# Performance work log

Hardware: AMD Instinct MI355X
Metric: run time of the kernel (lower is better)

Reference implementation:

```python
import jax, jax.numpy as jnp
import numpy as np

DIM = 256
HEADS = 8
HEAD_DIM = DIM // HEADS
EDGE_TYPES = 8  # edge_type_count; table has EDGE_TYPES+1 rows, row 0 is padding
B, N = 2, 2048
EPS = 1e-5


def layer_norm(x, g, b):
    mu = jnp.mean(x, axis=-1, keepdims=True)
    var = jnp.mean(jnp.square(x - mu), axis=-1, keepdims=True)
    return (x - mu) * jax.lax.rsqrt(var + EPS) * g + b


def setup_inputs() -> dict:
    key = jax.random.key(0)
    ks = jax.random.split(key, 12)
    s = 0.02
    x = jax.random.normal(ks[0], (B, N, DIM), dtype=jnp.float32)
    edge_types = jax.random.randint(ks[1], (B, N, N), 0, EDGE_TYPES + 1, dtype=jnp.int32)
    node_mask = jax.random.randint(ks[2], (B, N), 0, 2, dtype=jnp.int32).astype(bool)
    qkv_w = jax.random.normal(ks[3], (DIM, 3 * DIM), dtype=jnp.float32) * s
    qkv_b = jnp.zeros((3 * DIM,), jnp.float32)
    proj_w = jax.random.normal(ks[4], (DIM, DIM), dtype=jnp.float32) * s
    proj_b = jnp.zeros((DIM,), jnp.float32)
    edge_bias_table = jax.random.normal(ks[5], (EDGE_TYPES + 1, HEADS), dtype=jnp.float32) * s
    edge_bias_table = edge_bias_table.at[0].set(0.0)  # padding_idx=0
    ln1_g = jnp.ones((DIM,), jnp.float32); ln1_b = jnp.zeros((DIM,), jnp.float32)
    ln2_g = jnp.ones((DIM,), jnp.float32); ln2_b = jnp.zeros((DIM,), jnp.float32)
    ffn_w1 = jax.random.normal(ks[6], (DIM, 4 * DIM), dtype=jnp.float32) * s
    ffn_b1 = jnp.zeros((4 * DIM,), jnp.float32)
    ffn_w2 = jax.random.normal(ks[7], (4 * DIM, DIM), dtype=jnp.float32) * s
    ffn_b2 = jnp.zeros((DIM,), jnp.float32)
    return dict(x=x, edge_types=edge_types, node_mask=node_mask,
                qkv_w=qkv_w, qkv_b=qkv_b, proj_w=proj_w, proj_b=proj_b,
                edge_bias_table=edge_bias_table, ln1_g=ln1_g, ln1_b=ln1_b,
                ln2_g=ln2_g, ln2_b=ln2_b, ffn_w1=ffn_w1, ffn_b1=ffn_b1,
                ffn_w2=ffn_w2, ffn_b2=ffn_b2)


def reference(x, edge_types, node_mask, qkv_w, qkv_b, proj_w, proj_b,
              edge_bias_table, ln1_g, ln1_b, ln2_g, ln2_b,
              ffn_w1, ffn_b1, ffn_w2, ffn_b2):
    scale = HEAD_DIM ** -0.5
    residual = x
    h = layer_norm(x, ln1_g, ln1_b)
    qkv = h @ qkv_w + qkv_b                         # [B,N,3*DIM]
    qkv = qkv.reshape(B, N, 3, HEADS, HEAD_DIM)
    q, k, v = (qkv[:, :, 0].transpose(0, 2, 1, 3),  # [B,H,N,d]
               qkv[:, :, 1].transpose(0, 2, 1, 3),
               qkv[:, :, 2].transpose(0, 2, 1, 3))
    scores = jnp.einsum('bhnd,bhmd->bhnm', q, k) * scale
    bias = edge_bias_table[edge_types]              # [B,N,N,H]
    scores = scores + bias.transpose(0, 3, 1, 2)    # [B,H,N,N]
    eye = jnp.eye(N, dtype=bool)
    edge_mask = (edge_types != 0) | eye[None]
    node_mask_2d = node_mask[:, None, :] & node_mask[:, :, None]
    attn_mask = edge_mask & node_mask_2d            # [B,N,N]
    scores = jnp.where(attn_mask[:, None], scores, -1e9)
    attn = jax.nn.softmax(scores, axis=-1)
    out = jnp.einsum('bhnm,bhmd->bhnd', attn, v)
    out = out.transpose(0, 2, 1, 3).reshape(B, N, DIM)
    out = (out @ proj_w + proj_b) * node_mask[:, :, None]
    x1 = residual + out
    h2 = layer_norm(x1, ln2_g, ln2_b)
    h2 = jax.nn.gelu(h2 @ ffn_w1 + ffn_b1, approximate=False) @ ffn_w2 + ffn_b2
    h2 = h2 * node_mask[:, :, None]
    return x1 + h2
```

## Files before the change

### kernel.cpp

```cpp
#include <hip/hip_runtime.h>
#include <math.h>

#define DIMM 256
#define HEADS 8
#define NB 2048
#define BB 2
#define ROWS (BB*NB)

typedef __attribute__((ext_vector_type(8))) short bf16x8;
typedef __attribute__((ext_vector_type(4))) short bf16x4;
typedef __attribute__((ext_vector_type(4))) float f32x4;

__device__ inline unsigned short f2bf(float f) {
    unsigned int u = __float_as_uint(f);
    u += 0x7FFFu + ((u >> 16) & 1u);
    return (unsigned short)(u >> 16);
}
__device__ inline float bf2f(unsigned short u) {
    return __uint_as_float(((unsigned int)u) << 16);
}

__device__ inline int get_mask(const void* nm, int fmt, int idx) {
    if (fmt) return ((const unsigned char*)nm)[idx] != 0;
    return ((const int*)nm)[idx] != 0;
}

__global__ __launch_bounds__(256) void scan_w2bft_kernel(
    const void* __restrict__ nmask, int* __restrict__ nv,
    unsigned short* __restrict__ qidx,
    const float* __restrict__ w0, const float* __restrict__ w1,
    const float* __restrict__ w2, const float* __restrict__ w3,
    unsigned short* __restrict__ o0, unsigned short* __restrict__ o1,
    unsigned short* __restrict__ o2, unsigned short* __restrict__ o3)
{
    __shared__ float tile[64][65];
    __shared__ int fsh;
    __shared__ int cnt[256];
    int bid = blockIdx.x, t = threadIdx.x;
    if (bid < BB) {
        if (t == 0) fsh = 0;
        __syncthreads();
        if (((const unsigned char*)nmask)[4 * t + 1] != 0) fsh = 1;
        __syncthreads();
        int fm = fsh;
        int b = bid;
        int m[8]; int c = 0;
#pragma unroll
        for (int i = 0; i < 8; ++i) {
            m[i] = get_mask(nmask, fm, b * NB + t * 8 + i);
            c += m[i];
        }
        cnt[t] = c;
        __syncthreads();
#pragma unroll
        for (int off = 1; off < 256; off <<= 1) {
            int v = (t >= off) ? cnt[t - off] : 0;
            __syncthreads();
            cnt[t] += v;
            __syncthreads();
        }
        int mybase = cnt[t] - c;
        if (t == 255) nv[b] = cnt[255];
        int off = mybase;
#pragma unroll
        for (int i = 0; i < 8; ++i) {
            int row = t * 8 + i;
            if (m[i]) qidx[b * NB + off++] = (unsigned short)row;
        }
        __syncthreads();
        if (t == 0) {
            int n = cnt[255];
            unsigned short last = (n > 0) ? qidx[b * NB + n - 1] : (unsigned short)0;
            int padend = (n + 63) & ~63;
            for (int i = n; i < padend; ++i) qidx[b * NB + i] = last;
        }
    } else {
        int wb = bid - BB;
        const float* src; unsigned short* dst; int K, N, idx;
        if (wb < 48)       { src = w0; dst = o0; K = 256;  N = 768;  idx = wb; }
        else if (wb < 64)  { src = w1; dst = o1; K = 256;  N = 256;  idx = wb - 48; }
        else if (wb < 128) { src = w2; dst = o2; K = 256;  N = 1024; idx = wb - 64; }
        else               { src = w3; dst = o3; K = 1024; N = 256;  idx = wb - 128; }
        int ntiles = N >> 6;
        int k0 = (idx / ntiles) * 64, n0 = (idx % ntiles) * 64;
        int r = t >> 4, c4 = (t & 15) * 4;
#pragma unroll
        for (int i = 0; i < 4; ++i) {
            float4 v = *(const float4*)&src[(size_t)(k0 + r + i * 16) * N + n0 + c4];
            tile[r + i * 16][c4 + 0] = v.x;
            tile[r + i * 16][c4 + 1] = v.y;
            tile[r + i * 16][c4 + 2] = v.z;
            tile[r + i * 16][c4 + 3] = v.w;
        }
        __syncthreads();
#pragma unroll
        for (int i = 0; i < 4; ++i) {
            int n = n0 + r + i * 16;
            ushort4 u;
            u.x = f2bf(tile[c4 + 0][r + i * 16]);
            u.y = f2bf(tile[c4 + 1][r + i * 16]);
            u.z = f2bf(tile[c4 + 2][r + i * 16]);
            u.w = f2bf(tile[c4 + 3][r + i * 16]);
            *(ushort4*)&dst[(size_t)n * K + k0 + c4] = u;
        }
    }
}

__device__ inline void ln8_body(const float* __restrict__ x, const float* __restrict__ g,
                                const float* __restrict__ bb, unsigned short* __restrict__ o,
                                int xrow, int orow, int lane32) {
    int c0 = lane32 * 8;
    float4 v0 = *(const float4*)&x[(size_t)xrow * DIMM + c0];
    float4 v1 = *(const float4*)&x[(size_t)xrow * DIMM + c0 + 4];
    float s  = v0.x + v0.y + v0.z + v0.w + v1.x + v1.y + v1.z + v1.w;
    float s2 = v0.x*v0.x + v0.y*v0.y + v0.z*v0.z + v0.w*v0.w
             + v1.x*v1.x + v1.y*v1.y + v1.z*v1.z + v1.w*v1.w;
#pragma unroll
    for (int off = 16; off >= 1; off >>= 1) {
        s  += __shfl_xor(s,  off);
        s2 += __shfl_xor(s2, off);
    }
    float mean = s * (1.0f / DIMM);
    float var  = s2 * (1.0f / DIMM) - mean * mean;
    float rstd = rsqrtf(var + 1e-5f);
    float4 g0 = *(const float4*)&g[c0],  g1 = *(const float4*)&g[c0 + 4];
    float4 b0 = *(const float4*)&bb[c0], b1 = *(const float4*)&bb[c0 + 4];
    ushort4 u0, u1;
    u0.x = f2bf((v0.x - mean) * rstd * g0.x + b0.x);
    u0.y = f2bf((v0.y - mean) * rstd * g0.y + b0.y);
    u0.z = f2bf((v0.z - mean) * rstd * g0.z + b0.z);
    u0.w = f2bf((v0.w - mean) * rstd * g0.w + b0.w);
    u1.x = f2bf((v1.x - mean) * rstd * g1.x + b1.x);
    u1.y = f2bf((v1.y - mean) * rstd * g1.y + b1.y);
    u1.z = f2bf((v1.z - mean) * rstd * g1.z + b1.z);
    u1.w = f2bf((v1.w - mean) * rstd * g1.w + b1.w);
    *(ushort4*)&o[(size_t)orow * DIMM + c0]     = u0;
    *(ushort4*)&o[(size_t)orow * DIMM + c0 + 4] = u1;
}

__global__ __launch_bounds__(256) void prep_kernel(
    const float* __restrict__ x, const float* __restrict__ ln1_g,
    const float* __restrict__ ln1_b, unsigned short* __restrict__ h_ln,
    const int* __restrict__ etypes,
    unsigned char* __restrict__ emaskP,
    const int* __restrict__ nv, const unsigned short* __restrict__ qidx)
{
    __shared__ unsigned short kq[4][64];
    int bid = blockIdx.x, t = threadIdx.x;
    if (bid < 512) {
        int slotg = bid * 8 + (t >> 5);
        int b = slotg >> 11, sl = slotg & 2047;
        int nvp = (nv[b] + 63) & ~63;
        if (sl < nvp) {
            int row = qidx[b * NB + sl];
            ln8_body(x, ln1_g, ln1_b, h_ln, b * NB + row, slotg, t & 31);
        }
    } else {
        int wu = t >> 6;
        int unit = (bid - 512) * 4 + wu;
        int lane = t & 63, quad = lane >> 4, l15 = lane & 15;
        int b = unit >> 12;
        int qt16 = (unit >> 5) & 127;
        int kt = unit & 31;
        int nvb = nv[b];
        int nvp = (nvb + 63) & ~63;
        if (qt16 * 16 >= nvb || kt * 64 >= nvp) return;
        kq[wu][lane] = qidx[b * NB + kt * 64 + lane];
        int slot = qt16 * 16 + l15;
        int validq = slot < nvb;
        int qr = qidx[b * NB + slot];
        const int* erow = etypes + (size_t)(b * NB + qr) * NB;
        unsigned int dw[2] = {0u, 0u};
#pragma unroll
        for (int t16 = 0; t16 < 4; ++t16) {
            ushort4 ko = *(const ushort4*)&kq[wu][t16 * 16 + quad * 4];
            unsigned short kos[4] = {ko.x, ko.y, ko.z, ko.w};
#pragma unroll
            for (int r = 0; r < 4; ++r) {
                int ks = kt * 64 + t16 * 16 + quad * 4 + r;
                unsigned int code = 0u;
                if (validq && ks < nvb) {
                    int korig = kos[r];
                    int et = erow[korig];
                    if ((et != 0) || (korig == qr)) code = (unsigned int)(et + 1);
                }
                dw[t16 >> 1] |= code << ((t16 & 1) * 16 + r * 4);
            }
        }
        int2 o = {(int)dw[0], (int)dw[1]};
        *(int2*)(emaskP + (size_t)unit * 512 + lane * 8) = o;
    }
}

__global__ __launch_bounds__(256) void gemm_qkv_mfma(
    const unsigned short* __restrict__ A, const unsigned short* __restrict__ Bt,
    const float* __restrict__ bias, const int* __restrict__ nv,
    unsigned short* __restrict__ qkvh, unsigned short* __restrict__ vT)
{
    const int K = 256;
    int t = threadIdx.x, w = t >> 6, l = t & 63;
    int l15 = l & 15, quad = l >> 4;
    int n0 = blockIdx.x * 64;
    int m0c = blockIdx.y * 64;
    int b = blockIdx.z;
    int nvp = (nv[b] + 63) & ~63;
    if (m0c >= nvp) return;
    const unsigned short* ap = A + (size_t)(b * NB + m0c + w * 16 + l15) * K + quad * 8;
    const unsigned short* bp = Bt + (size_t)(n0 + l15) * K + quad * 8;

    f32x4 acc[4];
#pragma unroll
    for (int c = 0; c < 4; ++c) acc[c] = (f32x4){0.f, 0.f, 0.f, 0.f};

    bf16x8 aA, bA[4], aB, bB[4];
    auto ld = [&](bf16x8& af, bf16x8 (&bf)[4], int k0) {
        af = *(const bf16x8*)(ap + k0);
#pragma unroll
        for (int c = 0; c < 4; ++c)
            bf[c] = *(const bf16x8*)(bp + (size_t)(c * 16) * K + k0);
    };
    auto pr = [&](const bf16x8& af, const bf16x8 (&bf)[4]) {
#pragma unroll
        for (int c = 0; c < 4; ++c)
            acc[c] = __builtin_amdgcn_mfma_f32_16x16x32_bf16(af, bf[c], acc[c], 0, 0, 0);
    };
    ld(aA, bA, 0);
    for (int k0 = 0; k0 < K; k0 += 64) {
        ld(aB, bB, k0 + 32);
        pr(aA, bA);
        if (k0 + 64 < K) ld(aA, bA, k0 + 64);
        pr(aB, bB);
    }

    if (n0 < 512) {
        float sc = (n0 < 256) ? 0.17677669529663689f : 1.0f;
#pragma unroll
        for (int r = 0; r < 4; ++r) {
            int slot = b * NB + m0c + w * 16 + quad * 4 + r;
#pragma unroll
            for (int c = 0; c < 4; ++c) {
                int col = n0 + c * 16 + l15;
                qkvh[(size_t)slot * 512 + col] = f2bf((acc[c][r] + bias[col]) * sc);
            }
        }
    } else {
        int n = m0c + w * 16 + quad * 4;
#pragma unroll
        for (int c = 0; c < 4; ++c) {
            int col = n0 + c * 16 + l15 - 512;
            int hidx = col >> 5, d = col & 31;
            float bs = bias[n0 + c * 16 + l15];
            ushort4 u;
            u.x = f2bf(acc[c][0] + bs);
            u.y = f2bf(acc[c][1] + bs);
            u.z = f2bf(acc[c][2] + bs);
            u.w = f2bf(acc[c][3] + bs);
            *(ushort4*)&vT[(size_t)((b * HEADS + hidx) * 32 + d) * NB + n] = u;
        }
    }
}

__global__ __launch_bounds__(256) void attn_mfma(
    const unsigned short* __restrict__ qkvh,
    const unsigned short* __restrict__ vT,
    const unsigned char* __restrict__ emaskP,
    const float* __restrict__ table,
    const int* __restrict__ nv,
    unsigned short* __restrict__ OpH, float* __restrict__ lpart)
{
    __shared__ unsigned short P[4][16][72];
    __shared__ float tab2m[16];

    int t = threadIdx.x;
    int w = t >> 6, l = t & 63;
    int l15 = l & 15, quad = l >> 4;
    int h = blockIdx.x;
    int qt = blockIdx.y;
    int z = blockIdx.z, b = z >> 2, sp = z & 3;

    if (t < 16) tab2m[t] = (t >= 1 && t < 10) ? __expf(table[(t - 1) * 8 + h]) : 0.f;
    __syncthreads();

    int nvb = nv[b];
    int qt16 = qt * 4 + w;
    int q0c = qt16 * 16;
    if (q0c >= nvb) return;

    int nkt = (nvb + 63) >> 6;
    int tps = (nkt + 3) >> 2;
    int kbase = sp * tps * 64;
    int kend = min(kbase + tps * 64, nkt * 64);

    bf16x8 bq = *(const bf16x8*)(qkvh + (size_t)(b * NB + q0c + l15) * 512 + h * 32 + quad * 8);

    const unsigned short* kp = qkvh + (size_t)(b * NB + l15) * 512 + 256 + h * 32 + quad * 8;
    const unsigned short* vp = vT + (size_t)((b * HEADS + h) * 32 + l15) * NB + quad * 8;
    const unsigned char* ep = emaskP + (size_t)((b * 128 + qt16) * 32) * 512 + l * 8;

    float lacc = 0.f;
    f32x4 O0 = {0.f, 0.f, 0.f, 0.f}, O1 = {0.f, 0.f, 0.f, 0.f};

    bf16x8 kA[4], kB[4];
    bf16x8 vA[2][2], vB[2][2];
    int2 eA, eB;

    auto loadtile = [&](bf16x8 (&kf)[4], bf16x8 (&vf)[2][2], int2& ef, int m0) {
#pragma unroll
        for (int t16 = 0; t16 < 4; ++t16)
            kf[t16] = *(const bf16x8*)(kp + (size_t)(m0 + t16 * 16) * 512);
#pragma unroll
        for (int ks = 0; ks < 2; ++ks) {
            vf[ks][0] = *(const bf16x8*)(vp + m0 + ks * 32);
            vf[ks][1] = *(const bf16x8*)(vp + 16 * NB + m0 + ks * 32);
        }
        ef = *(const int2*)(ep + (size_t)(m0 >> 6) * 512);
    };

    auto process = [&](const bf16x8 (&kf)[4], const bf16x8 (&vf)[2][2], const int2& ef) {
#pragma unroll
        for (int t16 = 0; t16 < 4; ++t16) {
            f32x4 zero = {0.f, 0.f, 0.f, 0.f};
            f32x4 sT = __builtin_amdgcn_mfma_f32_16x16x32_bf16(kf[t16], bq, zero, 0, 0, 0);
            unsigned int e = ((unsigned int)((t16 < 2) ? ef.x : ef.y)) >> ((t16 & 1) * 16);
            float p0 = __expf(sT[0]) * tab2m[e & 0xFu];
            float p1 = __expf(sT[1]) * tab2m[(e >> 4) & 0xFu];
            float p2 = __expf(sT[2]) * tab2m[(e >> 8) & 0xFu];
            float p3 = __expf(sT[3]) * tab2m[(e >> 12) & 0xFu];
            lacc += (p0 + p1) + (p2 + p3);
            bf16x4 pb;
            pb[0] = (short)f2bf(p0); pb[1] = (short)f2bf(p1);
            pb[2] = (short)f2bf(p2); pb[3] = (short)f2bf(p3);
            *(bf16x4*)&P[w][l15][t16 * 16 + quad * 4] = pb;
        }
#pragma unroll
        for (int ks = 0; ks < 2; ++ks) {
            bf16x8 pa = *(const bf16x8*)&P[w][l15][ks * 32 + quad * 8];
            O0 = __builtin_amdgcn_mfma_f32_16x16x32_bf16(pa, vf[ks][0], O0, 0, 0, 0);
            O1 = __builtin_amdgcn_mfma_f32_16x16x32_bf16(pa, vf[ks][1], O1, 0, 0, 0);
        }
    };

    if (kbase < kend) {
        loadtile(kA, vA, eA, kbase);
        for (int m0 = kbase; m0 < kend; m0 += 128) {
            int n1 = (m0 + 64 < kend) ? m0 + 64 : kbase;
            loadtile(kB, vB, eB, n1);
            process(kA, vA, eA);
            if (m0 + 128 < kend) loadtile(kA, vA, eA, m0 + 128);
            if (m0 + 64 < kend) process(kB, vB, eB);
        }
    }

    lacc += __shfl_xor(lacc, 16);
    lacc += __shfl_xor(lacc, 32);

    unsigned short* Ob = OpH + (size_t)sp * ROWS * DIMM;
#pragma unroll
    for (int r = 0; r < 4; ++r) {
        int slot = q0c + quad * 4 + r;
        if (slot < nvb) {
            Ob[(size_t)(b * NB + slot) * DIMM + h * 32 + l15]      = f2bf(O0[r]);
            Ob[(size_t)(b * NB + slot) * DIMM + h * 32 + 16 + l15] = f2bf(O1[r]);
        }
    }
    if (quad == 0 && q0c + l15 < nvb)
        lpart[(size_t)sp * ROWS * 8 + (size_t)(b * NB + q0c + l15) * 8 + h] = lacc;
}

__global__ __launch_bounds__(1024) void megaback(
    const unsigned short* __restrict__ OpH, const float* __restrict__ lpart,
    const unsigned short* __restrict__ projT, const float* __restrict__ proj_b,
    const float* __restrict__ x, const void* __restrict__ nmask,
    const float* __restrict__ g2, const float* __restrict__ b2,
    const unsigned short* __restrict__ f1T, const float* __restrict__ ffn_b1,
    const unsigned short* __restrict__ f2T, const float* __restrict__ ffn_b2,
    const int* __restrict__ nv, const unsigned short* __restrict__ qidx,
    float* __restrict__ out)
{
    __shared__ float rinv_l[16][8];
    __shared__ float stats[16][2];
    __shared__ float redn[16][16][2];
    __shared__ unsigned short Astage[16][264];
    __shared__ float x1s[16][260];
    __shared__ unsigned short hstage[16][264];
    __shared__ unsigned short midstage[16][1032];
    __shared__ int fsh;

    int t = threadIdx.x;
    int bid = blockIdx.x;

    if (bid >= 256) {
        if (t == 0) fsh = 0;
        __syncthreads();
        if (((const unsigned char*)nmask)[4 * t + 1] != 0) fsh = 1;
        __syncthreads();
        int fm = fsh;
        int row = (bid - 256) * 32 + (t >> 5);
        if (!get_mask(nmask, fm, row)) {
            int c0 = (t & 31) * 8;
            float4 v0 = *(const float4*)&x[(size_t)row * DIMM + c0];
            float4 v1 = *(const float4*)&x[(size_t)row * DIMM + c0 + 4];
            *(float4*)&out[(size_t)row * DIMM + c0]     = v0;
            *(float4*)&out[(size_t)row * DIMM + c0 + 4] = v1;
        }
        return;
    }

    int w = t >> 6, l = t & 63;
    int l15 = l & 15, quad = l >> 4;
    int b = bid >> 7;
    int s0 = (bid & 127) * 16;
    int nvb = nv[b];
    if (s0 >= nvb) return;
    int slot0 = b * NB + s0;
    int col = w * 16 + l15;

    const unsigned short* bpp = projT + (size_t)col * 256 + quad * 8;
    bf16x8 psb[4];
#pragma unroll
    for (int i = 0; i < 4; ++i) psb[i] = *(const bf16x8*)(bpp + i * 32);

    if (t < 128) {
        int row = t >> 3, h = t & 7;
        float s = 0.f;
#pragma unroll
        for (int sp = 0; sp < 4; ++sp)
            s += lpart[(size_t)sp * ROWS * 8 + (size_t)(slot0 + row) * 8 + h];
        rinv_l[row][h] = (s > 0.f) ? 1.f / s : 0.f;
    }
    __syncthreads();

    {
        int row = t >> 6, col4 = (t & 63) * 4;
        float rinv = rinv_l[row][col4 >> 5];
        float o0 = 0.f, o1 = 0.f, o2 = 0.f, o3 = 0.f;
#pragma unroll
        for (int sp = 0; sp < 4; ++sp) {
            ushort4 u = *(const ushort4*)&OpH[(size_t)sp * ROWS * DIMM +
                                             (size_t)(slot0 + row) * DIMM + col4];
            o0 += bf2f(u.x); o1 += bf2f(u.y); o2 += bf2f(u.z); o3 += bf2f(u.w);
        }
        ushort4 u;
        u.x = f2bf(o0 * rinv); u.y = f2bf(o1 * rinv);
        u.z = f2bf(o2 * rinv); u.w = f2bf(o3 * rinv);
        *(ushort4*)&Astage[row][col4] = u;
    }
    __syncthreads();

    {
        f32x4 acc = (f32x4){0.f, 0.f, 0.f, 0.f};
#pragma unroll
        for (int ch = 0; ch < 8; ++ch) {
            bf16x8 a = *(const bf16x8*)&Astage[l15][ch * 32 + quad * 8];
            acc = __builtin_amdgcn_mfma_f32_16x16x32_bf16(a, psb[ch & 3], acc, 0, 0, 0);
            if (ch + 4 < 8) psb[ch & 3] = *(const bf16x8*)(bpp + (ch + 4) * 32);
        }
        float bs = proj_b[col];
#pragma unroll
        for (int r = 0; r < 4; ++r) {
            int row = quad * 4 + r;
            int grow = b * NB + qidx[(size_t)(slot0 + row)];
            float v = (acc[r] + bs) + x[(size_t)grow * DIMM + col];
            x1s[row][col] = v;
            float s = v, s2 = v * v;
#pragma unroll
            for (int off = 1; off < 16; off <<= 1) {
                s += __shfl_xor(s, off); s2 += __shfl_xor(s2, off);
            }
            if (l15 == 0) { redn[row][w][0] = s; redn[row][w][1] = s2; }
        }
    }
    const unsigned short* bpf1 = f1T + (size_t)(w * 64 + l15) * 256 + quad * 8;
    bf16x8 f1A[4];
#pragma unroll
    for (int c = 0; c < 4; ++c) f1A[c] = *(const bf16x8*)(bpf1 + (size_t)(c * 16) * 256);
    __syncthreads();
    if (t < 16) {
        float s = 0.f, s2 = 0.f;
#pragma unroll
        for (int ww = 0; ww < 16; ++ww) { s += redn[t][ww][0]; s2 += redn[t][ww][1]; }
        float mean = s * (1.f / DIMM);
        float var  = s2 * (1.f / DIMM) - mean * mean;
        stats[t][0] = mean; stats[t][1] = rsqrtf(var + 1e-5f);
    }
    __syncthreads();

    {
        float gv = g2[col], bv = b2[col];
#pragma unroll
        for (int r = 0; r < 4; ++r) {
            int row = quad * 4 + r;
            float hv = (x1s[row][col] - stats[row][0]) * stats[row][1] * gv + bv;
            hstage[row][col] = f2bf(hv);
        }
    }
    __syncthreads();

    {
        f32x4 acc[4];
#pragma unroll
        for (int c = 0; c < 4; ++c) acc[c] = (f32x4){0.f, 0.f, 0.f, 0.f};
        bf16x8 bB[4];
#pragma unroll
        for (int ch = 0; ch < 8; ++ch) {
            bf16x8 a = *(const bf16x8*)&hstage[l15][ch * 32 + quad * 8];
            if (ch + 1 < 8) {
#pragma unroll
                for (int c = 0; c < 4; ++c)
                    bB[c] = *(const bf16x8*)(bpf1 + (size_t)(c * 16) * 256 + (ch + 1) * 32);
            }
#pragma unroll
            for (int c = 0; c < 4; ++c)
                acc[c] = __builtin_amdgcn_mfma_f32_16x16x32_bf16(a, f1A[c], acc[c], 0, 0, 0);
#pragma unroll
            for (int c = 0; c < 4; ++c) f1A[c] = bB[c];
        }
#pragma unroll
        for (int c = 0; c < 4; ++c) {
            int colf = w * 64 + c * 16 + l15;
            float bs = ffn_b1[colf];
#pragma unroll
            for (int r = 0; r < 4; ++r) {
                float v = acc[c][r] + bs;
                float x2 = v * v;
                float p = v * fmaf(0.07135481f, x2, 1.5957691f);
                float e = __expf(p);
                float gl = v * (e / (e + 1.f));
                midstage[quad * 4 + r][colf] = f2bf(gl);
            }
        }
    }
    const unsigned short* bpf2 = f2T + (size_t)col * 1024 + quad * 8;
    bf16x8 f2sb[4];
#pragma unroll
    for (int i = 0; i < 4; ++i) f2sb[i] = *(const bf16x8*)(bpf2 + i * 32);
    __syncthreads();

    {
        f32x4 acc = (f32x4){0.f, 0.f, 0.f, 0.f};
#pragma unroll
        for (int ch = 0; ch < 32; ++ch) {
            bf16x8 a = *(const bf16x8*)&midstage[l15][ch * 32 + quad * 8];
            acc = __builtin_amdgcn_mfma_f32_16x16x32_bf16(a, f2sb[ch & 3], acc, 0, 0, 0);
            if (ch + 4 < 32) f2sb[ch & 3] = *(const bf16x8*)(bpf2 + (ch + 4) * 32);
        }
        float bs = ffn_b2[col];
#pragma unroll
        for (int r = 0; r < 4; ++r) {
            int row = quad * 4 + r;
            if (s0 + row < nvb) {
                int grow = b * NB + qidx[(size_t)(slot0 + row)];
                out[(size_t)grow * DIMM + col] = x1s[row][col] + (acc[r] + bs);
            }
        }
    }
}

extern "C" void kernel_launch(void* const* d_in, const int* in_sizes, int n_in,
                              void* d_out, int out_size, void* d_ws, size_t ws_size,
                              hipStream_t stream) {
    const float* x       = (const float*)d_in[0];
    const int*   etypes  = (const int*)d_in[1];
    const void*  nmask   = d_in[2];
    const float* qkv_w   = (const float*)d_in[3];
    const float* qkv_b   = (const float*)d_in[4];
    const float* proj_w  = (const float*)d_in[5];
    const float* proj_b  = (const float*)d_in[6];
    const float* table   = (const float*)d_in[7];
    const float* ln1_g   = (const float*)d_in[8];
    const float* ln1_b   = (const float*)d_in[9];
    const float* ln2_g   = (const float*)d_in[10];
    const float* ln2_b   = (const float*)d_in[11];
    const float* ffn_w1  = (const float*)d_in[12];
    const float* ffn_b1  = (const float*)d_in[13];
    const float* ffn_w2  = (const float*)d_in[14];
    const float* ffn_b2  = (const float*)d_in[15];
    float* out = (float*)d_out;
    float* ws  = (float*)d_ws;

    float* lpart = ws;
    unsigned short* ub = (unsigned short*)(ws + 131072);
    unsigned short* h_ln   = ub;
    unsigned short* qkvh   = ub + 1048576;
    unsigned short* vT     = ub + 3145728;
    unsigned short* OpH    = ub + 4194304;
    unsigned short* qkvT   = ub + 8388608;
    unsigned short* projT  = ub + 8585216;
    unsigned short* f1T    = ub + 8650752;
    unsigned short* f2T    = ub + 8912896;
    unsigned char* emaskP  = (unsigned char*)(ub + 9175040);
    unsigned short* qidx   = ub + 11272192;
    int* nv                = (int*)(ub + 11276288);

    scan_w2bft_kernel<<<dim3(BB + 192), dim3(256), 0, stream>>>(
        nmask, nv, qidx, qkv_w, proj_w, ffn_w1, ffn_w2, qkvT, projT, f1T, f2T);
    prep_kernel<<<dim3(2560), dim3(256), 0, stream>>>(
        x, ln1_g, ln1_b, h_ln, etypes, emaskP, nv, qidx);
    gemm_qkv_mfma<<<dim3(12, 32, BB), dim3(256), 0, stream>>>(h_ln, qkvT, qkv_b, nv, qkvh, vT);
    attn_mfma<<<dim3(HEADS, NB/64, BB*4), dim3(256), 0, stream>>>(
        qkvh, vT, emaskP, table, nv, OpH, lpart);
    megaback<<<dim3(256 + ROWS/32), dim3(1024), 0, stream>>>(
        OpH, lpart, projT, proj_b, x, nmask, ln2_g, ln2_b,
        f1T, ffn_b1, f2T, ffn_b2, nv, qidx, out);
}
```

Before: 193.6 us.

## Fuse LayerNorm1 into QKV GEMM and merge with edge-mask prep kernel

After: 191.7 us, median of 2. About the same (-1.0%).

```diff
diff --git a/kernel.cpp b/kernel.cpp
--- a/kernel.cpp
+++ b/kernel.cpp
@@ -106,58 +106,123 @@
     }
 }
 
-__device__ inline void ln8_body(const float* __restrict__ x, const float* __restrict__ g,
-                                const float* __restrict__ bb, unsigned short* __restrict__ o,
-                                int xrow, int orow, int lane32) {
-    int c0 = lane32 * 8;
-    float4 v0 = *(const float4*)&x[(size_t)xrow * DIMM + c0];
-    float4 v1 = *(const float4*)&x[(size_t)xrow * DIMM + c0 + 4];
-    float s  = v0.x + v0.y + v0.z + v0.w + v1.x + v1.y + v1.z + v1.w;
-    float s2 = v0.x*v0.x + v0.y*v0.y + v0.z*v0.z + v0.w*v0.w
-             + v1.x*v1.x + v1.y*v1.y + v1.z*v1.z + v1.w*v1.w;
-#pragma unroll
-    for (int off = 16; off >= 1; off >>= 1) {
-        s  += __shfl_xor(s,  off);
-        s2 += __shfl_xor(s2, off);
-    }
-    float mean = s * (1.0f / DIMM);
-    float var  = s2 * (1.0f / DIMM) - mean * mean;
-    float rstd = rsqrtf(var + 1e-5f);
-    float4 g0 = *(const float4*)&g[c0],  g1 = *(const float4*)&g[c0 + 4];
-    float4 b0 = *(const float4*)&bb[c0], b1 = *(const float4*)&bb[c0 + 4];
-    ushort4 u0, u1;
-    u0.x = f2bf((v0.x - mean) * rstd * g0.x + b0.x);
-    u0.y = f2bf((v0.y - mean) * rstd * g0.y + b0.y);
-    u0.z = f2bf((v0.z - mean) * rstd * g0.z + b0.z);
-    u0.w = f2bf((v0.w - mean) * rstd * g0.w + b0.w);
-    u1.x = f2bf((v1.x - mean) * rstd * g1.x + b1.x);
-    u1.y = f2bf((v1.y - mean) * rstd * g1.y + b1.y);
-    u1.z = f2bf((v1.z - mean) * rstd * g1.z + b1.z);
-    u1.w = f2bf((v1.w - mean) * rstd * g1.w + b1.w);
-    *(ushort4*)&o[(size_t)orow * DIMM + c0]     = u0;
-    *(ushort4*)&o[(size_t)orow * DIMM + c0 + 4] = u1;
-}
-
-__global__ __launch_bounds__(256) void prep_kernel(
+__global__ __launch_bounds__(256) void qkv_emask_kernel(
     const float* __restrict__ x, const float* __restrict__ ln1_g,
-    const float* __restrict__ ln1_b, unsigned short* __restrict__ h_ln,
+    const float* __restrict__ ln1_b,
+    const unsigned short* __restrict__ Bt, const float* __restrict__ bias,
     const int* __restrict__ etypes,
     unsigned char* __restrict__ emaskP,
-    const int* __restrict__ nv, const unsigned short* __restrict__ qidx)
+    const int* __restrict__ nv, const unsigned short* __restrict__ qidx,
+    unsigned short* __restrict__ qkvh, unsigned short* __restrict__ vT)
 {
+    __shared__ unsigned short Ah[64][264];
     __shared__ unsigned short kq[4][64];
     int bid = blockIdx.x, t = threadIdx.x;
-    if (bid < 512) {
-        int slotg = bid * 8 + (t >> 5);
-        int b = slotg >> 11, sl = slotg & 2047;
+    const int K = 256;
+
+    if (bid < 768) {
+        int q = bid;
+        int n0i = q % 12; q /= 12;
+        int m0i = q % 32;
+        int b = q / 32;
+        int n0 = n0i * 64;
+        int m0c = m0i * 64;
         int nvp = (nv[b] + 63) & ~63;
-        if (sl < nvp) {
-            int row = qidx[b * NB + sl];
-            ln8_body(x, ln1_g, ln1_b, h_ln, b * NB + row, slotg, t & 31);
+        if (m0c >= nvp) return;
+
+        for (int p = 0; p < 8; ++p) {
+            int lr = p * 8 + (t >> 5);
+            int lane32 = t & 31;
+            int row = qidx[b * NB + m0c + lr];
+            int c0 = lane32 * 8;
+            const float* xr = x + (size_t)(b * NB + row) * DIMM;
+            float4 v0 = *(const float4*)&xr[c0];
+            float4 v1 = *(const float4*)&xr[c0 + 4];
+            float s  = v0.x + v0.y + v0.z + v0.w + v1.x + v1.y + v1.z + v1.w;
+            float s2 = v0.x*v0.x + v0.y*v0.y + v0.z*v0.z + v0.w*v0.w
+                     + v1.x*v1.x + v1.y*v1.y + v1.z*v1.z + v1.w*v1.w;
+#pragma unroll
+            for (int off = 16; off >= 1; off >>= 1) {
+                s  += __shfl_xor(s,  off);
+                s2 += __shfl_xor(s2, off);
+            }
+            float mean = s * (1.0f / DIMM);
+            float var  = s2 * (1.0f / DIMM) - mean * mean;
+            float rstd = rsqrtf(var + 1e-5f);
+            float4 g0 = *(const float4*)&ln1_g[c0], g1 = *(const float4*)&ln1_g[c0 + 4];
+            float4 b0 = *(const float4*)&ln1_b[c0], b1 = *(const float4*)&ln1_b[c0 + 4];
+            ushort4 u0, u1;
+            u0.x = f2bf((v0.x - mean) * rstd * g0.x + b0.x);
+            u0.y = f2bf((v0.y - mean) * rstd * g0.y + b0.y);
+            u0.z = f2bf((v0.z - mean) * rstd * g0.z + b0.z);
+            u0.w = f2bf((v0.w - mean) * rstd * g0.w + b0.w);
+            u1.x = f2bf((v1.x - mean) * rstd * g1.x + b1.x);
+            u1.y = f2bf((v1.y - mean) * rstd * g1.y + b1.y);
+            u1.z = f2bf((v1.z - mean) * rstd * g1.z + b1.z);
+            u1.w = f2bf((v1.w - mean) * rstd * g1.w + b1.w);
+            *(ushort4*)&Ah[lr][c0]     = u0;
+            *(ushort4*)&Ah[lr][c0 + 4] = u1;
+        }
+        __syncthreads();
+
+        int w = t >> 6, l = t & 63;
+        int l15 = l & 15, quad = l >> 4;
+        const unsigned short* bp = Bt + (size_t)(n0 + l15) * K + quad * 8;
+        const unsigned short* alds = &Ah[w * 16 + l15][quad * 8];
+
+        f32x4 acc[4];
+#pragma unroll
+        for (int c = 0; c < 4; ++c) acc[c] = (f32x4){0.f, 0.f, 0.f, 0.f};
+
+        bf16x8 aA, bA[4], aB, bB[4];
+        auto ld = [&](bf16x8& af, bf16x8 (&bf)[4], int k0) {
+            af = *(const bf16x8*)(alds + k0);
+#pragma unroll
+            for (int c = 0; c < 4; ++c)
+                bf[c] = *(const bf16x8*)(bp + (size_t)(c * 16) * K + k0);
+        };
+        auto pr = [&](const bf16x8& af, const bf16x8 (&bf)[4]) {
+#pragma unroll
+            for (int c = 0; c < 4; ++c)
+                acc[c] = __builtin_amdgcn_mfma_f32_16x16x32_bf16(af, bf[c], acc[c], 0, 0, 0);
+        };
+        ld(aA, bA, 0);
+        for (int k0 = 0; k0 < K; k0 += 64) {
+            ld(aB, bB, k0 + 32);
+            pr(aA, bA);
+            if (k0 + 64 < K) ld(aA, bA, k0 + 64);
+            pr(aB, bB);
+        }
+
+        if (n0 < 512) {
+            float sc = (n0 < 256) ? 0.17677669529663689f : 1.0f;
+#pragma unroll
+            for (int r = 0; r < 4; ++r) {
+                int slot = b * NB + m0c + w * 16 + quad * 4 + r;
+#pragma unroll
+                for (int c = 0; c < 4; ++c) {
+                    int col = n0 + c * 16 + l15;
+                    qkvh[(size_t)slot * 512 + col] = f2bf((acc[c][r] + bias[col]) * sc);
+                }
+            }
+        } else {
+            int n = m0c + w * 16 + quad * 4;
+#pragma unroll
+            for (int c = 0; c < 4; ++c) {
+                int col = n0 + c * 16 + l15 - 512;
+                int hidx = col >> 5, d = col & 31;
+                float bs = bias[n0 + c * 16 + l15];
+                ushort4 u;
+                u.x = f2bf(acc[c][0] + bs);
+                u.y = f2bf(acc[c][1] + bs);
+                u.z = f2bf(acc[c][2] + bs);
+                u.w = f2bf(acc[c][3] + bs);
+                *(ushort4*)&vT[(size_t)((b * HEADS + hidx) * 32 + d) * NB + n] = u;
+            }
         }
     } else {
         int wu = t >> 6;
-        int unit = (bid - 512) * 4 + wu;
+        int unit = (bid - 768) * 4 + wu;
         int lane = t & 63, quad = lane >> 4, l15 = lane & 15;
         int b = unit >> 12;
         int qt16 = (unit >> 5) & 127;
@@ -189,74 +254,6 @@
         }
         int2 o = {(int)dw[0], (int)dw[1]};
         *(int2*)(emaskP + (size_t)unit * 512 + lane * 8) = o;
-    }
-}
-
-__global__ __launch_bounds__(256) void gemm_qkv_mfma(
-    const unsigned short* __restrict__ A, const unsigned short* __restrict__ Bt,
-    const float* __restrict__ bias, const int* __restrict__ nv,
-    unsigned short* __restrict__ qkvh, unsigned short* __restrict__ vT)
-{
-    const int K = 256;
-    int t = threadIdx.x, w = t >> 6, l = t & 63;
-    int l15 = l & 15, quad = l >> 4;
-    int n0 = blockIdx.x * 64;
-    int m0c = blockIdx.y * 64;
-    int b = blockIdx.z;
-    int nvp = (nv[b] + 63) & ~63;
-    if (m0c >= nvp) return;
-    const unsigned short* ap = A + (size_t)(b * NB + m0c + w * 16 + l15) * K + quad * 8;
-    const unsigned short* bp = Bt + (size_t)(n0 + l15) * K + quad * 8;
-
-    f32x4 acc[4];
-#pragma unroll
-    for (int c = 0; c < 4; ++c) acc[c] = (f32x4){0.f, 0.f, 0.f, 0.f};
-
-    bf16x8 aA, bA[4], aB, bB[4];
-    auto ld = [&](bf16x8& af, bf16x8 (&bf)[4], int k0) {
-        af = *(const bf16x8*)(ap + k0);
-#pragma unroll
-        for (int c = 0; c < 4; ++c)
-            bf[c] = *(const bf16x8*)(bp + (size_t)(c * 16) * K + k0);
-    };
-    auto pr = [&](const bf16x8& af, const bf16x8 (&bf)[4]) {
-#pragma unroll
-        for (int c = 0; c < 4; ++c)
-            acc[c] = __builtin_amdgcn_mfma_f32_16x16x32_bf16(af, bf[c], acc[c], 0, 0, 0);
-    };
-    ld(aA, bA, 0);
-    for (int k0 = 0; k0 < K; k0 += 64) {
-        ld(aB, bB, k0 + 32);
-        pr(aA, bA);
-        if (k0 + 64 < K) ld(aA, bA, k0 + 64);
-        pr(aB, bB);
-    }
-
-    if (n0 < 512) {
-        float sc = (n0 < 256) ? 0.17677669529663689f : 1.0f;
-#pragma unroll
-        for (int r = 0; r < 4; ++r) {
-            int slot = b * NB + m0c + w * 16 + quad * 4 + r;
-#pragma unroll
-            for (int c = 0; c < 4; ++c) {
-                int col = n0 + c * 16 + l15;
-                qkvh[(size_t)slot * 512 + col] = f2bf((acc[c][r] + bias[col]) * sc);
-            }
-        }
-    } else {
-        int n = m0c + w * 16 + quad * 4;
-#pragma unroll
-        for (int c = 0; c < 4; ++c) {
-            int col = n0 + c * 16 + l15 - 512;
-            int hidx = col >> 5, d = col & 31;
-            float bs = bias[n0 + c * 16 + l15];
-            ushort4 u;
-            u.x = f2bf(acc[c][0] + bs);
-            u.y = f2bf(acc[c][1] + bs);
-            u.z = f2bf(acc[c][2] + bs);
-            u.w = f2bf(acc[c][3] + bs);
-            *(ushort4*)&vT[(size_t)((b * HEADS + hidx) * 32 + d) * NB + n] = u;
-        }
     }
 }
 
@@ -580,7 +577,6 @@
 
     float* lpart = ws;
     unsigned short* ub = (unsigned short*)(ws + 131072);
-    unsigned short* h_ln   = ub;
     unsigned short* qkvh   = ub + 1048576;
     unsigned short* vT     = ub + 3145728;
     unsigned short* OpH    = ub + 4194304;
@@ -594,9 +590,8 @@
 
     scan_w2bft_kernel<<<dim3(BB + 192), dim3(256), 0, stream>>>(
         nmask, nv, qidx, qkv_w, proj_w, ffn_w1, ffn_w2, qkvT, projT, f1T, f2T);
-    prep_kernel<<<dim3(2560), dim3(256), 0, stream>>>(
-        x, ln1_g, ln1_b, h_ln, etypes, emaskP, nv, qidx);
-    gemm_qkv_mfma<<<dim3(12, 32, BB), dim3(256), 0, stream>>>(h_ln, qkvT, qkv_b, nv, qkvh, vT);
+    qkv_emask_kernel<<<dim3(768 + 2048), dim3(256), 0, stream>>>(
+        x, ln1_g, ln1_b, qkvT, qkv_b, etypes, emaskP, nv, qidx, qkvh, vT);
     attn_mfma<<<dim3(HEADS, NB/64, BB*4), dim3(256), 0, stream>>>(
         qkvh, vT, emaskP, table, nv, OpH, lpart);
     megaback<<<dim3(256 + ROWS/32), dim3(1024), 0, stream>>>(
```
